# Kernel optimization log

Hardware: AMD Instinct MI355X
Metric: run time of the kernel (lower is better)

Reference implementation:

```python
import jax, jax.numpy as jnp
import numpy as np

H, DH, C, K = 8, 128, 200, 15  # heads, head_dim, context_size, conv kernel
SCALE = DH ** -0.5
EPS = 1e-5


def layernorm(x, g, b):
    mu = jnp.mean(x, axis=-1, keepdims=True)
    var = jnp.mean(jnp.square(x - mu), axis=-1, keepdims=True)
    return (x - mu) * jax.lax.rsqrt(var + EPS) * g + b


def feedforward(x, ln_g, ln_b, up_w, up_b, down_w, down_b):
    h = layernorm(x, ln_g, ln_b)
    h = jax.nn.silu(h @ up_w + up_b)
    return h @ down_w + down_b


def attention(x, dist, ln_g, ln_b, wq, wkv, wo, wo_b, rel_emb):
    h = layernorm(x, ln_g, ln_b)
    b, f, d = h.shape
    nb = f // C  # num_features chosen divisible by context_size (no remainder path)
    q = (h @ wq).reshape(b, nb, C, H, DH).transpose(0, 1, 3, 2, 4)   # [b,nb,H,C,dh]
    kv = h @ wkv
    k, v = jnp.split(kv, 2, axis=-1)
    k = k.reshape(b, nb, C, H, DH).transpose(0, 1, 3, 2, 4)
    v = v.reshape(b, nb, C, H, DH).transpose(0, 1, 3, 2, 4)
    rel = rel_emb[dist]                                              # [C,C,dh]
    pos_attn = jnp.einsum('bnhid,ijd->bnhij', q, rel) * SCALE
    scores = jnp.einsum('bnhid,bnhjd->bnhij', q, k) * SCALE + pos_attn
    probs = jax.nn.softmax(scores, axis=-1)
    out = jnp.einsum('bnhij,bnhjd->bnhid', probs, v)
    out = out.transpose(0, 1, 3, 2, 4).reshape(b, f, H * DH)
    return out @ wo + wo_b


def conv_module(x, ln_g, ln_b, up_w, up_b, dw_w, bn_g, bn_b, bn_mean, bn_var, down_w, down_b):
    h = layernorm(x, ln_g, ln_b)
    h = h @ up_w + up_b                         # pointwise conv == linear; [b,L,2*inner]
    a, gate = jnp.split(h, 2, axis=-1)
    h = a * jax.nn.sigmoid(gate)                # GLU over channel dim
    h = h.transpose(0, 2, 1)                    # [b,inner,L]
    pad = K // 2
    h = jax.lax.conv_general_dilated(
        h, dw_w[:, None, :], window_strides=(1,), padding=[(pad, pad)],
        dimension_numbers=('NCH', 'OIH', 'NCH'), feature_group_count=h.shape[1])
    # BatchNorm1d in eval mode (running stats)
    h = (h - bn_mean[None, :, None]) * jax.lax.rsqrt(bn_var[None, :, None] + EPS)
    h = h * bn_g[None, :, None] + bn_b[None, :, None]
    h = jax.nn.silu(h)
    h = h.transpose(0, 2, 1) @ down_w + down_b  # [b,L,hidden]
    return h


def block_forward(x, attention_dists,
                  ff1_ln_g, ff1_ln_b, ff1_up_w, ff1_up_b, ff1_down_w, ff1_down_b,
                  attn_ln_g, attn_ln_b, wq, wkv, wo, wo_b, rel_emb,
                  conv_ln_g, conv_ln_b, conv_up_w, conv_up_b, dw_w,
                  bn_g, bn_b, bn_mean, bn_var, conv_down_w, conv_down_b,
                  ff2_ln_g, ff2_ln_b, ff2_up_w, ff2_up_b, ff2_down_w, ff2_down_b,
                  post_ln_g, post_ln_b):
    x = 0.5 * feedforward(x, ff1_ln_g, ff1_ln_b, ff1_up_w, ff1_up_b, ff1_down_w, ff1_down_b) + x
    x = attention(x, attention_dists, attn_ln_g, attn_ln_b, wq, wkv, wo, wo_b, rel_emb) + x
    x = conv_module(x, conv_ln_g, conv_ln_b, conv_up_w, conv_up_b, dw_w,
                    bn_g, bn_b, bn_mean, bn_var, conv_down_w, conv_down_b) + x
    x = 0.5 * feedforward(x, ff2_ln_g, ff2_ln_b, ff2_up_w, ff2_up_b, ff2_down_w, ff2_down_b) + x
    return layernorm(x, post_ln_g, post_ln_b)


def setup_inputs() -> dict:
    key = jax.random.key(0)
    ks = iter(jax.random.split(key, 40))
    d, dff, inner = 1024, 4096, 2048
    r = lambda shape, s=0.02: (jax.random.normal(next(ks), shape, jnp.float32) * s)
    inp = {
        'x': jax.random.normal(next(ks), (8, 2000, d), jnp.float32),
        'attention_dists': jax.random.randint(next(ks), (C, C), 0, 1025, jnp.int32),
        'ff1_ln_g': jnp.ones((d,)), 'ff1_ln_b': jnp.zeros((d,)),
        'ff1_up_w': r((d, dff)), 'ff1_up_b': jnp.zeros((dff,)),
        'ff1_down_w': r((dff, d)), 'ff1_down_b': jnp.zeros((d,)),
        'attn_ln_g': jnp.ones((d,)), 'attn_ln_b': jnp.zeros((d,)),
        'wq': r((d, H * DH)), 'wkv': r((d, 2 * H * DH)),
        'wo': r((H * DH, d)), 'wo_b': jnp.zeros((d,)),
        'rel_emb': r((2 * 512 + 1, DH)),
        'conv_ln_g': jnp.ones((d,)), 'conv_ln_b': jnp.zeros((d,)),
        'conv_up_w': r((d, 2 * inner)), 'conv_up_b': jnp.zeros((2 * inner,)),
        'dw_w': r((inner, K)),
        'bn_g': jnp.ones((inner,)), 'bn_b': jnp.zeros((inner,)),
        'bn_mean': r((inner,)), 'bn_var': jax.random.uniform(next(ks), (inner,), jnp.float32) + 0.5,
        'conv_down_w': r((inner, d)), 'conv_down_b': jnp.zeros((d,)),
        'ff2_ln_g': jnp.ones((d,)), 'ff2_ln_b': jnp.zeros((d,)),
        'ff2_up_w': r((d, dff)), 'ff2_up_b': jnp.zeros((dff,)),
        'ff2_down_w': r((dff, d)), 'ff2_down_b': jnp.zeros((d,)),
        'post_ln_g': jnp.ones((d,)), 'post_ln_b': jnp.zeros((d,)),
    }
    return inp


def reference(x, attention_dists,
              ff1_ln_g, ff1_ln_b, ff1_up_w, ff1_up_b, ff1_down_w, ff1_down_b,
              attn_ln_g, attn_ln_b, wq, wkv, wo, wo_b, rel_emb,
              conv_ln_g, conv_ln_b, conv_up_w, conv_up_b, dw_w,
              bn_g, bn_b, bn_mean, bn_var, conv_down_w, conv_down_b,
              ff2_ln_g, ff2_ln_b, ff2_up_w, ff2_up_b, ff2_down_w, ff2_down_b,
              post_ln_g, post_ln_b):
    return block_forward(x, attention_dists,
                         ff1_ln_g, ff1_ln_b, ff1_up_w, ff1_up_b, ff1_down_w, ff1_down_b,
                         attn_ln_g, attn_ln_b, wq, wkv, wo, wo_b, rel_emb,
                         conv_ln_g, conv_ln_b, conv_up_w, conv_up_b, dw_w,
                         bn_g, bn_b, bn_mean, bn_var, conv_down_w, conv_down_b,
                         ff2_ln_g, ff2_ln_b, ff2_up_w, ff2_up_b, ff2_down_w, ff2_down_b,
                         post_ln_g, post_ln_b)
```

## Files before the change

### kernel.cpp

```cpp
#include <hip/hip_runtime.h>

typedef unsigned short u16;
typedef unsigned int u32;
using short8 = __attribute__((ext_vector_type(8))) short;
using floatx4 = __attribute__((ext_vector_type(4))) float;

#define DMODEL 1024
#define DFF 4096
#define INNER 2048
#define DH 128
#define CTX 200
#define R_TOT 16000
#define ABN 40
#define AROWS (ABN * CTX)
#define AM (ABN * 8)
#define SCALE_Q 0.08838834764831845f

__device__ __forceinline__ u16 f2bf(float f) {
    union { float f; u32 u; } v; v.f = f;
    u32 r = v.u + 0x7FFFu + ((v.u >> 16) & 1u);
    return (u16)(r >> 16);
}
__device__ __forceinline__ float bf2f(u16 u) {
    union { u32 u; float f; } v; v.u = ((u32)u) << 16; return v.f;
}
__device__ __forceinline__ float sigmoidf_(float x) { return 1.f / (1.f + __expf(-x)); }

__device__ __forceinline__ void load_lds16(const void* g, void* l) {
    __builtin_amdgcn_global_load_lds((const __attribute__((address_space(1))) u32*)g,
                                     (__attribute__((address_space(3))) u32*)l, 16, 0, 0);
}

template <typename RowMap>
__device__ __forceinline__ void stage_half(const char* __restrict__ src, RowMap rowoff,
                                           int nrows, int row0, int k0b, char* slab, int half) {
    const int lane = threadIdx.x & 63;
    const int wave = threadIdx.x >> 6;
#pragma unroll
    for (int r = 2 * half; r < 2 * half + 2; ++r) {
        int o = r * 8192 + wave * 1024 + lane * 16;
        int row = o >> 7;
        int srcb = (o & 127) ^ ((row & 7) << 4);
        int grow = row0 + row;
        grow = (grow < nrows) ? grow : (nrows - 1);
        load_lds16(src + rowoff(grow) + k0b + srcb, slab + r * 8192 + wave * 1024);
    }
}

template <typename RMA, typename RMB, typename Epi>
__device__ __forceinline__ void gemm256_core(const char* __restrict__ A, RMA rma, int a_rows,
                                             const char* __restrict__ B, RMB rmb, int b_rows,
                                             int K, int row0, int col0, char* lds, Epi epi) {
    char* ldsA = lds;
    char* ldsB = lds + 65536;
    const int lane = threadIdx.x & 63;
    const int wave = threadIdx.x >> 6;
    const int wrow = (wave >> 2) * 128;
    const int wcol = (wave & 3) * 64;
    const int lr = lane & 15;
    const int kg = lane >> 4;
    const int nt = K >> 6;

    floatx4 acc[8][4];
#pragma unroll
    for (int i = 0; i < 8; ++i)
#pragma unroll
        for (int j = 0; j < 4; ++j) acc[i][j] = (floatx4){0.f, 0.f, 0.f, 0.f};

    stage_half(B, rmb, b_rows, col0, 0, ldsB, 0);
    stage_half(B, rmb, b_rows, col0, 0, ldsB, 1);
    stage_half(A, rma, a_rows, row0, 0, ldsA, 0);
    stage_half(A, rma, a_rows, row0, 0, ldsA, 1);
    if (nt > 1) {
        stage_half(B, rmb, b_rows, col0, 128, ldsB + 32768, 0);
        stage_half(B, rmb, b_rows, col0, 128, ldsB + 32768, 1);
    }

    int bcur = 0;
    for (int t = 0; t < nt; ++t) {
        char* curA = ldsA + (t & 1) * 32768;
        char* curB = ldsB + bcur * 32768;
        const int bnx2 = (bcur >= 1) ? bcur - 1 : 2;
        if (t + 1 < nt)
            asm volatile("s_waitcnt vmcnt(4)" ::: "memory");
        else
            asm volatile("s_waitcnt vmcnt(0)" ::: "memory");
        __builtin_amdgcn_s_barrier();

        short8 bv[4][2];
#pragma unroll
        for (int ni = 0; ni < 4; ++ni) {
            int row = wcol + ni * 16 + lr;
#pragma unroll
            for (int ks = 0; ks < 2; ++ks) {
                int cb = (ks * 64 + kg * 16) ^ ((row & 7) << 4);
                bv[ni][ks] = *(const short8*)(curB + row * 128 + cb);
            }
        }
#pragma unroll
        for (int q = 0; q < 4; ++q) {
            short8 av[2][2];
#pragma unroll
            for (int m2 = 0; m2 < 2; ++m2) {
                int row = wrow + (2 * q + m2) * 16 + lr;
#pragma unroll
                for (int ks = 0; ks < 2; ++ks) {
                    int cb = (ks * 64 + kg * 16) ^ ((row & 7) << 4);
                    av[m2][ks] = *(const short8*)(curA + row * 128 + cb);
                }
            }
            if (q == 0 && t + 1 < nt)
                stage_half(A, rma, a_rows, row0, (t + 1) << 7, ldsA + ((t + 1) & 1) * 32768, 0);
            if (q == 1 && t + 1 < nt)
                stage_half(A, rma, a_rows, row0, (t + 1) << 7, ldsA + ((t + 1) & 1) * 32768, 1);
            if (q == 2 && t + 2 < nt)
                stage_half(B, rmb, b_rows, col0, (t + 2) << 7, ldsB + bnx2 * 32768, 0);
            if (q == 3 && t + 2 < nt)
                stage_half(B, rmb, b_rows, col0, (t + 2) << 7, ldsB + bnx2 * 32768, 1);
            asm volatile("s_waitcnt lgkmcnt(0)" ::: "memory");
            __builtin_amdgcn_sched_barrier(0);
            __builtin_amdgcn_s_setprio(1);
#pragma unroll
            for (int ks = 0; ks < 2; ++ks)
#pragma unroll
                for (int m2 = 0; m2 < 2; ++m2)
#pragma unroll
                    for (int ni = 0; ni < 4; ++ni)
                        acc[2 * q + m2][ni] = __builtin_amdgcn_mfma_f32_16x16x32_bf16(
                            av[m2][ks], bv[ni][ks], acc[2 * q + m2][ni], 0, 0, 0);
            __builtin_amdgcn_s_setprio(0);
            __builtin_amdgcn_s_barrier();
        }
        bcur = (bcur >= 2) ? 0 : bcur + 1;
    }
#pragma unroll
    for (int mi = 0; mi < 8; ++mi)
#pragma unroll
        for (int ni = 0; ni < 4; ++ni)
#pragma unroll
            for (int rr = 0; rr < 4; ++rr)
                epi(row0 + wrow + mi * 16 + kg * 4 + rr, col0 + wcol + ni * 16 + lr,
                    acc[mi][ni][rr]);
}

__device__ __forceinline__ void xcd_stripe_remap(int& bx, int& by) {
    const int gx = gridDim.x;
    const int gxs = gx >> 3;
    const int id = blockIdx.y * gx + blockIdx.x;
    const int xcd = id & 7;
    const int local = id >> 3;
    bx = xcd * gxs + (local % gxs);
    by = local / gxs;
}

template <int MODE>
__global__ __launch_bounds__(512, 2) void k_gemm256(const u16* __restrict__ A, int lda,
                                                    const u16* __restrict__ Bt, int ldb,
                                                    const float* __restrict__ bias, float alpha,
                                                    void* out, int ldc, const float* resid,
                                                    int M, int N, int K) {
    __shared__ __align__(128) char lds[163840];
    int bx, by;
    xcd_stripe_remap(bx, by);
    const int row0 = bx * 256, col0 = by * 256;
    if (row0 >= M) return;
    u16* ob = (u16*)out;
    float* of = (float*)out;
    const size_t la = (size_t)lda * 2, lb = (size_t)ldb * 2;
    gemm256_core((const char*)A, [=](int r) { return (size_t)r * la; }, M,
                 (const char*)Bt, [=](int r) { return (size_t)r * lb; }, N, K, row0, col0, lds,
                 [&](int r, int c, float v) {
                     if (r >= M) return;
                     size_t idx = (size_t)r * ldc + c;
                     float bb = bias ? bias[c] : 0.f;
                     if (MODE == 0) {
                         ob[idx] = f2bf(alpha * v + bb);
                     } else if (MODE == 1) {
                         float t = v + bb;
                         ob[idx] = f2bf(t * sigmoidf_(t));
                     } else {
                         of[idx] = alpha * (v + bb) + resid[idx];
                     }
                 });
}

template <typename RowMap>
__device__ __forceinline__ void stage_tile_g(const char* __restrict__ src, RowMap rowoff,
                                             int nrows, int row0, int k0b, char* tile) {
    const int lane = threadIdx.x & 63;
    const int wave = threadIdx.x >> 6;
#pragma unroll
    for (int r = 0; r < 4; ++r) {
        int o = r * 4096 + wave * 1024 + lane * 16;
        int row = o >> 7;
        int srcb = (o & 127) ^ ((row & 7) << 4);
        int grow = row0 + row;
        grow = (grow < nrows) ? grow : (nrows - 1);
        const char* g = src + rowoff(grow) + k0b + srcb;
        load_lds16(g, tile + r * 4096 + wave * 1024);
    }
}

template <typename RMA, typename RMB, typename Epi>
__device__ __forceinline__ void gemm_core_g(const char* __restrict__ A, RMA rma, int a_rows,
                                            const char* __restrict__ B, RMB rmb, int b_rows,
                                            int K, int row0, int col0, char* lds, Epi epi) {
    const int lane = threadIdx.x & 63;
    const int wave = threadIdx.x >> 6;
    const int wrow = (wave >> 1) * 64;
    const int wcol = (wave & 1) * 64;
    const int lr = lane & 15;
    const int kg = lane >> 4;
    const int nt = K >> 6;

    floatx4 acc[4][4];
#pragma unroll
    for (int i = 0; i < 4; ++i)
#pragma unroll
        for (int j = 0; j < 4; ++j) acc[i][j] = (floatx4){0.f, 0.f, 0.f, 0.f};

    stage_tile_g(A, rma, a_rows, row0, 0, lds);
    stage_tile_g(B, rmb, b_rows, col0, 0, lds + 16384);
    asm volatile("s_waitcnt vmcnt(0)" ::: "memory");
    __builtin_amdgcn_s_barrier();

    for (int t = 0; t < nt; ++t) {
        char* cur = lds + (t & 1) * 32768;
        char* nxt = lds + ((t + 1) & 1) * 32768;
        if (t + 1 < nt) {
            stage_tile_g(A, rma, a_rows, row0, (t + 1) << 7, nxt);
            stage_tile_g(B, rmb, b_rows, col0, (t + 1) << 7, nxt + 16384);
        }
#pragma unroll
        for (int ks = 0; ks < 2; ++ks) {
            short8 av[4], bv[4];
#pragma unroll
            for (int mi = 0; mi < 4; ++mi) {
                int row = wrow + mi * 16 + lr;
                int cb = (ks * 64 + kg * 16) ^ ((row & 7) << 4);
                av[mi] = *(const short8*)(cur + row * 128 + cb);
            }
#pragma unroll
            for (int ni = 0; ni < 4; ++ni) {
                int row = wcol + ni * 16 + lr;
                int cb = (ks * 64 + kg * 16) ^ ((row & 7) << 4);
                bv[ni] = *(const short8*)(cur + 16384 + row * 128 + cb);
            }
            __builtin_amdgcn_s_setprio(1);
#pragma unroll
            for (int mi = 0; mi < 4; ++mi)
#pragma unroll
                for (int ni = 0; ni < 4; ++ni)
                    acc[mi][ni] = __builtin_amdgcn_mfma_f32_16x16x32_bf16(av[mi], bv[ni],
                                                                          acc[mi][ni], 0, 0, 0);
            __builtin_amdgcn_s_setprio(0);
        }
        if (t + 1 < nt)
            asm volatile("s_waitcnt vmcnt(0) lgkmcnt(0)" ::: "memory");
        else
            asm volatile("s_waitcnt lgkmcnt(0)" ::: "memory");
        __builtin_amdgcn_sched_barrier(0);
        __builtin_amdgcn_s_barrier();
    }
#pragma unroll
    for (int mi = 0; mi < 4; ++mi)
#pragma unroll
        for (int ni = 0; ni < 4; ++ni)
#pragma unroll
            for (int rr = 0; rr < 4; ++rr)
                epi(row0 + wrow + mi * 16 + kg * 4 + rr, col0 + wcol + ni * 16 + lr,
                    acc[mi][ni][rr]);
}

__global__ __launch_bounds__(256, 2) void k_qk(const u16* __restrict__ q,
                                               const u16* __restrict__ kvc,
                                               u16* __restrict__ sc, int bn0) {
    __shared__ __align__(128) char lds[65536];
    const int z = blockIdx.z, bnl = z >> 3, h = z & 7;
    const char* A = (const char*)(q + ((size_t)(bn0 + bnl) * CTX) * DMODEL + h * DH);
    const char* B = (const char*)(kvc + ((size_t)bnl * CTX) * (2 * DMODEL) + h * DH);
    u16* out = sc + (size_t)z * CTX * 256;
    gemm_core_g(A, [](int r) { return (size_t)r * (DMODEL * 2); }, CTX, B,
                [](int r) { return (size_t)r * (4 * DMODEL); }, CTX, DH, blockIdx.x * 128,
                blockIdx.y * 128, lds, [&](int r, int c, float v) {
                    if (r < CTX) out[(size_t)r * 256 + c] = f2bf(v);
                });
}

__global__ __launch_bounds__(256, 2) void k_pos(const u16* __restrict__ q,
                                                const u16* __restrict__ rel,
                                                u16* __restrict__ sc, int m0) {
    __shared__ __align__(128) char lds[65536];
    const int i = blockIdx.z;
    const char* B = (const char*)(rel + (size_t)i * CTX * DH);
    u16* out = sc + i * 256;
    gemm_core_g((const char*)q,
                [=](int r) {
                    int m = m0 + r;
                    return (size_t)(((m >> 3) * CTX + i) * DMODEL + (m & 7) * DH) * 2;
                },
                AM, B, [](int r) { return (size_t)r * (DH * 2); }, CTX, DH, blockIdx.x * 128,
                blockIdx.y * 128, lds, [&](int r, int c, float v) {
                    if (r < AM) {
                        size_t idx = (size_t)r * (CTX * 256) + c;
                        out[idx] = f2bf(bf2f(out[idx]) + v);
                    }
                });
}

__global__ __launch_bounds__(256, 2) void k_pv(const u16* __restrict__ P,
                                               const u16* __restrict__ vT,
                                               u16* __restrict__ attn, int bn0) {
    __shared__ __align__(128) char lds[65536];
    const int z = blockIdx.z;
    u16* out = attn + ((size_t)(bn0 + (z >> 3)) * CTX) * DMODEL + (z & 7) * DH;
    const char* A = (const char*)(P + (size_t)z * CTX * 256);
    const char* B = (const char*)(vT + (size_t)z * DH * 256);
    gemm_core_g(A, [](int r) { return (size_t)r * 512; }, CTX, B,
                [](int r) { return (size_t)r * 512; }, DH, 256, blockIdx.x * 128, 0, lds,
                [&](int r, int c, float v) {
                    if (r < CTX) out[(size_t)r * DMODEL + c] = f2bf(v);
                });
}

template <bool OUTF32>
__global__ __launch_bounds__(256) void k_ln(const float* __restrict__ x,
                                            const float* __restrict__ g,
                                            const float* __restrict__ b, void* __restrict__ out) {
    const int row = blockIdx.x, t = threadIdx.x, lane = t & 63, wv = t >> 6;
    const float4 v = ((const float4*)(x + (size_t)row * DMODEL))[t];
    float s = v.x + v.y + v.z + v.w;
    float q = v.x * v.x + v.y * v.y + v.z * v.z + v.w * v.w;
#pragma unroll
    for (int off = 32; off > 0; off >>= 1) { s += __shfl_down(s, off); q += __shfl_down(q, off); }
    __shared__ float rs_[4], rq_[4];
    if (lane == 0) { rs_[wv] = s; rq_[wv] = q; }
    __syncthreads();
    s = rs_[0] + rs_[1] + rs_[2] + rs_[3];
    q = rq_[0] + rq_[1] + rq_[2] + rq_[3];
    const float mu = s * (1.f / DMODEL);
    const float rstd = rsqrtf(q * (1.f / DMODEL) - mu * mu + 1e-5f);
    const float4 gv = ((const float4*)g)[t];
    const float4 bv = ((const float4*)b)[t];
    float o0 = (v.x - mu) * rstd * gv.x + bv.x;
    float o1 = (v.y - mu) * rstd * gv.y + bv.y;
    float o2 = (v.z - mu) * rstd * gv.z + bv.z;
    float o3 = (v.w - mu) * rstd * gv.w + bv.w;
    if (OUTF32) {
        ((float4*)out)[(size_t)row * 256 + t] = make_float4(o0, o1, o2, o3);
    } else {
        ushort4 r4;
        r4.x = f2bf(o0); r4.y = f2bf(o1); r4.z = f2bf(o2); r4.w = f2bf(o3);
        ((ushort4*)out)[(size_t)row * 256 + t] = r4;
    }
}

__global__ __launch_bounds__(256) void k_softmax(u16* __restrict__ sc) {
    const size_t row = blockIdx.x;
    const int t = threadIdx.x, lane = t & 63, wv = t >> 6;
    float v = (t < CTX) ? bf2f(sc[row * 256 + t]) : -3.0e38f;
    float m = v;
#pragma unroll
    for (int off = 32; off > 0; off >>= 1) m = fmaxf(m, __shfl_down(m, off));
    __shared__ float rm[4], rsum[4];
    if (lane == 0) rm[wv] = m;
    __syncthreads();
    m = fmaxf(fmaxf(rm[0], rm[1]), fmaxf(rm[2], rm[3]));
    float e = (t < CTX) ? __expf(v - m) : 0.f;
    float s = e;
#pragma unroll
    for (int off = 32; off > 0; off >>= 1) s += __shfl_down(s, off);
    if (lane == 0) rsum[wv] = s;
    __syncthreads();
    s = rsum[0] + rsum[1] + rsum[2] + rsum[3];
    sc[row * 256 + t] = f2bf(e / s);
}

__global__ __launch_bounds__(256) void k_glu(u16* __restrict__ mid) {
    const size_t r = blockIdx.x;
    const int c = threadIdx.x * 8;
    const short8 a8 = *(const short8*)(mid + r * 4096 + c);
    const short8 g8 = *(const short8*)(mid + r * 4096 + 2048 + c);
    short8 o8;
#pragma unroll
    for (int e = 0; e < 8; ++e) {
        float av = bf2f((u16)a8[e]), gg = bf2f((u16)g8[e]);
        o8[e] = (short)f2bf(av * sigmoidf_(gg));
    }
    *(short8*)(mid + r * 4096 + c) = o8;
}

__global__ __launch_bounds__(256) void k_dwconv(const u16* __restrict__ in,
                                                const float* __restrict__ w,
                                                const float* __restrict__ bng,
                                                const float* __restrict__ bnb,
                                                const float* __restrict__ bnm,
                                                const float* __restrict__ bnv,
                                                u16* __restrict__ out) {
    const int b = blockIdx.z, lt = blockIdx.x, cg = blockIdx.y;
    const int c = cg * 256 + threadIdx.x;
    const int l0 = lt * 16;
    __shared__ u16 s[30][256];
#pragma unroll
    for (int rr = 0; rr < 30; ++rr) {
        int l = l0 + rr - 7;
        u16 v = 0;
        if (l >= 0 && l < 2000) v = in[((size_t)b * 2000 + l) * 4096 + c];
        s[rr][threadIdx.x] = v;
    }
    __syncthreads();
    float wv[15];
#pragma unroll
    for (int k = 0; k < 15; ++k) wv[k] = w[c * 15 + k];
    const float sc = rsqrtf(bnv[c] + 1e-5f) * bng[c];
    const float mean = bnm[c], bb = bnb[c];
#pragma unroll
    for (int l = 0; l < 16; ++l) {
        float acc = 0.f;
#pragma unroll
        for (int k = 0; k < 15; ++k) acc += bf2f(s[l + k][threadIdx.x]) * wv[k];
        float h = (acc - mean) * sc + bb;
        h = h * sigmoidf_(h);
        out[((size_t)b * 2000 + l0 + l) * 4096 + c] = f2bf(h);
    }
}

__global__ __launch_bounds__(256) void k_wt(const float* __restrict__ w, u16* __restrict__ wt,
                                            int K, int N) {
    __shared__ float tile[32][33];
    const int k0 = blockIdx.x * 32, n0 = blockIdx.y * 32;
    const int tx = threadIdx.x & 31, ty = threadIdx.x >> 5;
#pragma unroll
    for (int i = 0; i < 32; i += 8) tile[ty + i][tx] = w[(size_t)(k0 + ty + i) * N + n0 + tx];
    __syncthreads();
#pragma unroll
    for (int i = 0; i < 32; i += 8)
        wt[(size_t)(n0 + ty + i) * K + k0 + tx] = f2bf(tile[tx][ty + i]);
}

__global__ void k_rel(const float* __restrict__ emb, const int* __restrict__ dist,
                      u16* __restrict__ rel) {
    const int bid = blockIdx.x;
    const int d = dist[bid];
    rel[(size_t)bid * DH + threadIdx.x] = f2bf(emb[(size_t)d * DH + threadIdx.x]);
}

__global__ __launch_bounds__(256) void k_vt(const u16* __restrict__ kvc, u16* __restrict__ vT) {
    __shared__ u16 t_[64 * 130];
    const int z = blockIdx.x, jt = blockIdx.y;
    const int bnl = z >> 3, h = z & 7;
    const int j0 = jt * 64;
    for (int idx = threadIdx.x; idx < 8192; idx += 256) {
        int j = idx >> 7, dh = idx & 127;
        int jj = j0 + j;
        u16 val = 0;
        if (jj < CTX) val = kvc[((size_t)(bnl * CTX + jj)) * (2 * DMODEL) + DMODEL + h * DH + dh];
        t_[j * 130 + dh] = val;
    }
    __syncthreads();
    for (int idx = threadIdx.x; idx < 8192; idx += 256) {
        int dh = idx >> 6, j = idx & 63;
        vT[((size_t)z * DH + dh) * 256 + j0 + j] = t_[j * 130 + dh];
    }
}

__global__ void k_fill(float* o, int n, float v) {
    int i = blockIdx.x * 256 + threadIdx.x;
    if (i < n) o[i] = v;
}

extern "C" void kernel_launch(void* const* d_in, const int* in_sizes, int n_in, void* d_out,
                              int out_size, void* d_ws, size_t ws_size, hipStream_t stream) {
    const float* x_in = (const float*)d_in[0];
    const int* dists = (const int*)d_in[1];
    const float* ff1_ln_g = (const float*)d_in[2];
    const float* ff1_ln_b = (const float*)d_in[3];
    const float* ff1_up_w = (const float*)d_in[4];
    const float* ff1_up_b = (const float*)d_in[5];
    const float* ff1_down_w = (const float*)d_in[6];
    const float* ff1_down_b = (const float*)d_in[7];
    const float* attn_ln_g = (const float*)d_in[8];
    const float* attn_ln_b = (const float*)d_in[9];
    const float* wq = (const float*)d_in[10];
    const float* wkv = (const float*)d_in[11];
    const float* wo = (const float*)d_in[12];
    const float* wo_b = (const float*)d_in[13];
    const float* rel_emb = (const float*)d_in[14];
    const float* conv_ln_g = (const float*)d_in[15];
    const float* conv_ln_b = (const float*)d_in[16];
    const float* conv_up_w = (const float*)d_in[17];
    const float* conv_up_b = (const float*)d_in[18];
    const float* dw_w = (const float*)d_in[19];
    const float* bn_g = (const float*)d_in[20];
    const float* bn_b = (const float*)d_in[21];
    const float* bn_mean = (const float*)d_in[22];
    const float* bn_var = (const float*)d_in[23];
    const float* conv_down_w = (const float*)d_in[24];
    const float* conv_down_b = (const float*)d_in[25];
    const float* ff2_ln_g = (const float*)d_in[26];
    const float* ff2_ln_b = (const float*)d_in[27];
    const float* ff2_up_w = (const float*)d_in[28];
    const float* ff2_up_b = (const float*)d_in[29];
    const float* ff2_down_w = (const float*)d_in[30];
    const float* ff2_down_b = (const float*)d_in[31];
    const float* post_ln_g = (const float*)d_in[32];
    const float* post_ln_b = (const float*)d_in[33];

    char* W = (char*)d_ws;
    size_t off = 0;
    auto alloc = [&](size_t bytes) {
        char* p = W + off;
        off += (bytes + 255) & ~(size_t)255;
        return (u16*)p;
    };
    u16* slot = alloc((size_t)4096 * 1024 * 2);
    u16* ln_buf = alloc((size_t)R_TOT * DMODEL * 2);
    u16* arena = alloc((size_t)R_TOT * DFF * 2);
    u16* mid = arena;
    u16* rel_bf = arena;
    u16* bufA = rel_bf + (size_t)CTX * CTX * DH;
    u16* bufB = bufA + (size_t)AROWS * 2 * DMODEL;
    u16* smid = bufB + (size_t)R_TOT * DMODEL;
    u16* vT = smid + (size_t)AM * CTX * 256;
    float* xs = (float*)d_out;

    if (ws_size < off) {
        k_fill<<<(out_size + 255) / 256, 256, 0, stream>>>((float*)d_out, out_size, 31337.f);
        return;
    }

    auto WT = [&](const float* s, int K, int N) {
        k_wt<<<dim3(K / 32, N / 32), 256, 0, stream>>>(s, slot, K, N);
    };

    const dim3 gUP(64, 16);
    const dim3 gSQ(64, 4);
    const dim3 gKV(32, 8);

    auto ff_block = [&](const float* lng, const float* lnb, const float* upw, const float* upb,
                        const float* dnw, const float* dnb, const float* resid,
                        const float* xsrc) {
        k_ln<false><<<R_TOT, 256, 0, stream>>>(xsrc, lng, lnb, ln_buf);
        WT(upw, 1024, 4096);
        k_gemm256<1><<<gUP, 512, 0, stream>>>(ln_buf, DMODEL, slot, DMODEL, upb, 1.f, mid, DFF,
                                              nullptr, R_TOT, DFF, DMODEL);
        WT(dnw, 4096, 1024);
        k_gemm256<2><<<gSQ, 512, 0, stream>>>(mid, DFF, slot, DFF, dnb, 0.5f, xs, DMODEL, resid,
                                              R_TOT, DMODEL, DFF);
    };

    ff_block(ff1_ln_g, ff1_ln_b, ff1_up_w, ff1_up_b, ff1_down_w, ff1_down_b, x_in, x_in);

    k_ln<false><<<R_TOT, 256, 0, stream>>>(xs, attn_ln_g, attn_ln_b, ln_buf);
    k_rel<<<CTX * CTX, 128, 0, stream>>>(rel_emb, dists, rel_bf);
    WT(wq, 1024, 1024);
    k_gemm256<0><<<gSQ, 512, 0, stream>>>(ln_buf, DMODEL, slot, DMODEL, nullptr, SCALE_Q, bufB,
                                          DMODEL, nullptr, R_TOT, DMODEL, DMODEL);
    WT(wkv, 1024, 2048);
    for (int h = 0; h < 2; ++h) {
        const int bn0 = h * ABN, m0 = bn0 * 8;
        const u16* lnc = ln_buf + (size_t)bn0 * CTX * DMODEL;
        k_gemm256<0><<<gKV, 512, 0, stream>>>(lnc, DMODEL, slot, DMODEL, nullptr, 1.f, bufA,
                                              2 * DMODEL, nullptr, AROWS, 2 * DMODEL, DMODEL);
        k_vt<<<dim3(AM, 4), 256, 0, stream>>>(bufA, vT);
        k_qk<<<dim3(2, 2, AM), 256, 0, stream>>>(bufB, bufA, smid, bn0);
        k_pos<<<dim3(3, 2, CTX), 256, 0, stream>>>(bufB, rel_bf, smid, m0);
        k_softmax<<<AM * CTX, 256, 0, stream>>>(smid);
        k_pv<<<dim3(2, 1, AM), 256, 0, stream>>>(smid, vT, bufB, bn0);
    }
    WT(wo, 1024, 1024);
    k_gemm256<2><<<gSQ, 512, 0, stream>>>(bufB, DMODEL, slot, DMODEL, wo_b, 1.f, xs, DMODEL, xs,
                                          R_TOT, DMODEL, DMODEL);

    k_ln<false><<<R_TOT, 256, 0, stream>>>(xs, conv_ln_g, conv_ln_b, ln_buf);
    WT(conv_up_w, 1024, 4096);
    k_gemm256<0><<<gUP, 512, 0, stream>>>(ln_buf, DMODEL, slot, DMODEL, conv_up_b, 1.f, mid, DFF,
                                          nullptr, R_TOT, DFF, DMODEL);
    k_glu<<<R_TOT, 256, 0, stream>>>(mid);
    k_dwconv<<<dim3(125, 8, 8), 256, 0, stream>>>(mid, dw_w, bn_g, bn_b, bn_mean, bn_var,
                                                  mid + INNER);
    WT(conv_down_w, 2048, 1024);
    k_gemm256<2><<<gSQ, 512, 0, stream>>>(mid + INNER, DFF, slot, INNER, conv_down_b, 1.f, xs,
                                          DMODEL, xs, R_TOT, DMODEL, INNER);

    ff_block(ff2_ln_g, ff2_ln_b, ff2_up_w, ff2_up_b, ff2_down_w, ff2_down_b, xs, xs);

    k_ln<true><<<R_TOT, 256, 0, stream>>>(xs, post_ln_g, post_ln_b, d_out);
}
```

Measured before the change: 1.940 ms.

## Replace triple-buffered B staging with symmetric double-buffered A/B pipeline in GEMM

Result: no change. 1.963 ms (+1.2%).

```diff
diff --git a/kernel.cpp b/kernel.cpp
--- a/kernel.cpp
+++ b/kernel.cpp
@@ -33,17 +33,17 @@
 
 template <typename RowMap>
 __device__ __forceinline__ void stage_half(const char* __restrict__ src, RowMap rowoff,
-                                           int nrows, int row0, int k0b, char* slab, int half) {
+                                           int nrows, int grow0, int k0b, char* dst16k) {
     const int lane = threadIdx.x & 63;
     const int wave = threadIdx.x >> 6;
 #pragma unroll
-    for (int r = 2 * half; r < 2 * half + 2; ++r) {
+    for (int r = 0; r < 2; ++r) {
         int o = r * 8192 + wave * 1024 + lane * 16;
         int row = o >> 7;
         int srcb = (o & 127) ^ ((row & 7) << 4);
-        int grow = row0 + row;
+        int grow = grow0 + row;
         grow = (grow < nrows) ? grow : (nrows - 1);
-        load_lds16(src + rowoff(grow) + k0b + srcb, slab + r * 8192 + wave * 1024);
+        load_lds16(src + rowoff(grow) + k0b + srcb, dst16k + r * 8192 + wave * 1024);
     }
 }
 
@@ -51,8 +51,6 @@
 __device__ __forceinline__ void gemm256_core(const char* __restrict__ A, RMA rma, int a_rows,
                                              const char* __restrict__ B, RMB rmb, int b_rows,
                                              int K, int row0, int col0, char* lds, Epi epi) {
-    char* ldsA = lds;
-    char* ldsB = lds + 65536;
     const int lane = threadIdx.x & 63;
     const int wave = threadIdx.x >> 6;
     const int wrow = (wave >> 2) * 128;
@@ -67,38 +65,31 @@
 #pragma unroll
         for (int j = 0; j < 4; ++j) acc[i][j] = (floatx4){0.f, 0.f, 0.f, 0.f};
 
-    stage_half(B, rmb, b_rows, col0, 0, ldsB, 0);
-    stage_half(B, rmb, b_rows, col0, 0, ldsB, 1);
-    stage_half(A, rma, a_rows, row0, 0, ldsA, 0);
-    stage_half(A, rma, a_rows, row0, 0, ldsA, 1);
-    if (nt > 1) {
-        stage_half(B, rmb, b_rows, col0, 128, ldsB + 32768, 0);
-        stage_half(B, rmb, b_rows, col0, 128, ldsB + 32768, 1);
-    }
-
-    int bcur = 0;
+    stage_half(A, rma, a_rows, row0, 0, lds);
+    stage_half(A, rma, a_rows, row0 + 128, 0, lds + 16384);
+    stage_half(B, rmb, b_rows, col0, 0, lds + 32768);
+    stage_half(B, rmb, b_rows, col0 + 128, 0, lds + 49152);
+    asm volatile("s_waitcnt vmcnt(0)" ::: "memory");
+    __builtin_amdgcn_s_barrier();
+
     for (int t = 0; t < nt; ++t) {
-        char* curA = ldsA + (t & 1) * 32768;
-        char* curB = ldsB + bcur * 32768;
-        const int bnx2 = (bcur >= 1) ? bcur - 1 : 2;
-        if (t + 1 < nt)
-            asm volatile("s_waitcnt vmcnt(4)" ::: "memory");
-        else
-            asm volatile("s_waitcnt vmcnt(0)" ::: "memory");
-        __builtin_amdgcn_s_barrier();
-
+        char* cur = lds + (t & 1) * 65536;
+        char* nxt = lds + ((t + 1) & 1) * 65536;
+        const int k1b = (t + 1) << 7;
         short8 bv[4][2];
 #pragma unroll
-        for (int ni = 0; ni < 4; ++ni) {
-            int row = wcol + ni * 16 + lr;
-#pragma unroll
-            for (int ks = 0; ks < 2; ++ks) {
-                int cb = (ks * 64 + kg * 16) ^ ((row & 7) << 4);
-                bv[ni][ks] = *(const short8*)(curB + row * 128 + cb);
+        for (int q = 0; q < 4; ++q) {
+            if (q == 0) {
+#pragma unroll
+                for (int ni = 0; ni < 4; ++ni) {
+                    int row = wcol + ni * 16 + lr;
+#pragma unroll
+                    for (int ks = 0; ks < 2; ++ks) {
+                        int cb = (ks * 64 + kg * 16) ^ ((row & 7) << 4);
+                        bv[ni][ks] = *(const short8*)(cur + 32768 + row * 128 + cb);
+                    }
+                }
             }
-        }
-#pragma unroll
-        for (int q = 0; q < 4; ++q) {
             short8 av[2][2];
 #pragma unroll
             for (int m2 = 0; m2 < 2; ++m2) {
@@ -106,17 +97,16 @@
 #pragma unroll
                 for (int ks = 0; ks < 2; ++ks) {
                     int cb = (ks * 64 + kg * 16) ^ ((row & 7) << 4);
-                    av[m2][ks] = *(const short8*)(curA + row * 128 + cb);
+                    av[m2][ks] = *(const short8*)(cur + row * 128 + cb);
                 }
             }
-            if (q == 0 && t + 1 < nt)
-                stage_half(A, rma, a_rows, row0, (t + 1) << 7, ldsA + ((t + 1) & 1) * 32768, 0);
-            if (q == 1 && t + 1 < nt)
-                stage_half(A, rma, a_rows, row0, (t + 1) << 7, ldsA + ((t + 1) & 1) * 32768, 1);
-            if (q == 2 && t + 2 < nt)
-                stage_half(B, rmb, b_rows, col0, (t + 2) << 7, ldsB + bnx2 * 32768, 0);
-            if (q == 3 && t + 2 < nt)
-                stage_half(B, rmb, b_rows, col0, (t + 2) << 7, ldsB + bnx2 * 32768, 1);
+            if (t + 1 < nt) {
+                if (q == 0) stage_half(A, rma, a_rows, row0, k1b, nxt);
+                if (q == 1) stage_half(A, rma, a_rows, row0 + 128, k1b, nxt + 16384);
+                if (q == 2) stage_half(B, rmb, b_rows, col0, k1b, nxt + 32768);
+                if (q == 3) stage_half(B, rmb, b_rows, col0 + 128, k1b, nxt + 49152);
+            }
+            __builtin_amdgcn_s_barrier();
             asm volatile("s_waitcnt lgkmcnt(0)" ::: "memory");
             __builtin_amdgcn_sched_barrier(0);
             __builtin_amdgcn_s_setprio(1);
@@ -129,9 +119,10 @@
                         acc[2 * q + m2][ni] = __builtin_amdgcn_mfma_f32_16x16x32_bf16(
                             av[m2][ks], bv[ni][ks], acc[2 * q + m2][ni], 0, 0, 0);
             __builtin_amdgcn_s_setprio(0);
+            if (q == 3 && t + 1 < nt)
+                asm volatile("s_waitcnt vmcnt(0)" ::: "memory");
             __builtin_amdgcn_s_barrier();
         }
-        bcur = (bcur >= 2) ? 0 : bcur + 1;
     }
 #pragma unroll
     for (int mi = 0; mi < 8; ++mi)
@@ -159,7 +150,7 @@
                                                     const float* __restrict__ bias, float alpha,
                                                     void* out, int ldc, const float* resid,
                                                     int M, int N, int K) {
-    __shared__ __align__(128) char lds[163840];
+    __shared__ __align__(128) char lds[131072];
     int bx, by;
     xcd_stripe_remap(bx, by);
     const int row0 = bx * 256, col0 = by * 256;
```
